# Optimization experiments

Hardware: AMD Instinct MI355X
Metric: run time of the kernel (lower is better)

The kernel has to match this reference:

```python
import jax, jax.numpy as jnp
import numpy as np

H = 2048

def setup_inputs() -> dict:
    key = jax.random.key(0)
    ks = jax.random.split(key, 7)
    s = 1.0 / np.sqrt(H)
    return {
        "input": jax.random.normal(ks[0], (2, 4096, H), dtype=jnp.float32),
        "Wq": jax.random.uniform(ks[1], (H, H), jnp.float32, -s, s),
        "bq": jax.random.uniform(ks[2], (H,), jnp.float32, -s, s),
        "Wk": jax.random.uniform(ks[3], (H, H), jnp.float32, -s, s),
        "bk": jax.random.uniform(ks[4], (H,), jnp.float32, -s, s),
        "Wv": jax.random.uniform(ks[5], (H, H), jnp.float32, -s, s),
        "bv": jax.random.uniform(ks[6], (H,), jnp.float32, -s, s),
    }

def reference(input, Wq, bq, Wk, bk, Wv, bv):
    # Linear projections: y = x @ W^T + b (torch nn.Linear convention)
    q = jnp.einsum('bsh,oh->bso', input, Wq) + bq
    k = jnp.einsum('bsh,oh->bso', input, Wk) + bk
    v = jnp.einsum('bsh,oh->bso', input, Wv) + bv
    # NOTE: original module has NO 1/sqrt(d) scaling and NO mask
    scores = jnp.einsum('bqh,bkh->bqk', q, k)          # [B,S,S]
    attn = jax.nn.softmax(scores, axis=-1)
    out = jnp.einsum('bqk,bkh->bqh', attn, v)           # [B,S,H]
    return out
```

## Files before the change

kernel.cpp:

```cpp
#include <hip/hip_runtime.h>
#include <hip/hip_bf16.h>
#include <cstdint>
#include <cstddef>


typedef _Float16 half8 __attribute__((ext_vector_type(8)));
typedef _Float16 half4 __attribute__((ext_vector_type(4)));
typedef float    f32x4 __attribute__((ext_vector_type(4)));

__device__ __forceinline__ void gld_lds16(const void* g, void* l) {
  __builtin_amdgcn_global_load_lds(
      (const __attribute__((address_space(1))) unsigned int*)g,
      (__attribute__((address_space(3))) unsigned int*)l, 16, 0, 0);
}

#define FENCE()  asm volatile("" ::: "memory")
#define LGKM(n)  asm volatile("s_waitcnt lgkmcnt(" #n ")" ::: "memory")
#define VMC(n)   asm volatile("s_waitcnt vmcnt(" #n ")" ::: "memory")
#define SBAR()   do { __builtin_amdgcn_s_barrier(); FENCE(); } while (0)
#define SCHED0() __builtin_amdgcn_sched_barrier(0)
#define PRIO1()  __builtin_amdgcn_s_setprio(1)
#define PRIO0()  __builtin_amdgcn_s_setprio(0)

#define LOAD_A(dst, RB, MH) do {                                            \
  const char* _p = ldsA + ((RB)*2 + wr) * 16384 + fr * 128;                 \
  _Pragma("unroll") for (int mi = 0; mi < 4; ++mi) {                        \
    dst[mi][0] = *(const half8*)(_p + ((MH)*4 + mi) * 2048 + cS0);          \
    dst[mi][1] = *(const half8*)(_p + ((MH)*4 + mi) * 2048 + cS1);          \
  }                                                                         \
} while (0)

#define LOAD_B(dst, RB, NH) do {                                            \
  const char* _p = ldsB + ((RB)*2 + (wc >> 1)) * 16384 +                    \
                   ((wc & 1) * 64 + fr) * 128;                              \
  _Pragma("unroll") for (int ni = 0; ni < 2; ++ni) {                        \
    dst[ni][0] = *(const half8*)(_p + ((NH)*2 + ni) * 2048 + cS0);          \
    dst[ni][1] = *(const half8*)(_p + ((NH)*2 + ni) * 2048 + cS1);          \
  }                                                                         \
} while (0)

#define MFMA_Q(AF, BF, MH, NH)                                              \
  _Pragma("unroll") for (int mi = 0; mi < 4; ++mi)                          \
  _Pragma("unroll") for (int ni = 0; ni < 2; ++ni) {                        \
    f32x4& _c = acc[(MH)*4 + mi][(NH)*2 + ni];                              \
    _c = __builtin_amdgcn_mfma_f32_16x16x32_f16(AF[mi][0], BF[ni][0], _c, 0, 0, 0); \
    _c = __builtin_amdgcn_mfma_f32_16x16x32_f16(AF[mi][1], BF[ni][1], _c, 0, 0, 0); \
  }

#define STAGE_A(bsel, h, kof)                                               \
  {                                                                         \
    const _Float16* _s = Abase + (size_t)((h) * 128) * lda + (kof);         \
    char* _d = ldsA + ((bsel)*2 + (h)) * 16384 + wvd;                       \
    gld_lds16(_s, _d);                                                      \
    gld_lds16(_s + lda8, _d + 1024);                                        \
  }
#define STAGE_B(bsel, h, kof)                                               \
  {                                                                         \
    const _Float16* _s = Bbase + (size_t)((h) * 128) * ldb + (kof);         \
    char* _d = ldsB + ((bsel)*2 + (h)) * 16384 + wvd;                       \
    gld_lds16(_s, _d);                                                      \
    gld_lds16(_s + ldb8, _d + 1024);                                        \
  }

template <int MODE>
__global__ __launch_bounds__(512) void gemm256(
    const _Float16* __restrict__ A, int lda,
    const _Float16* __restrict__ B, int ldb,
    const float* __restrict__ bias,
    void* __restrict__ out, int ldo, int K,
    size_t sA, size_t sB, size_t sO)
{
  __shared__ __attribute__((aligned(128))) char lds[131072];
  char* ldsA = (char*)lds;
  char* ldsB = (char*)lds + 65536;

  const int tid  = threadIdx.x;
  const int wv   = tid >> 6;
  const int lane = tid & 63;
  const int wr = wv >> 2;
  const int wc = wv & 3;
  const int bm = blockIdx.x * 256;
  const int bn = blockIdx.y * 256;
  A += (size_t)blockIdx.z * sA;
  B += (size_t)blockIdx.z * sB;

  const int fr = lane & 15;
  const int kq = lane >> 4;
  const int sx = (fr & 7) << 4;
  const int cS0 = (kq * 16) ^ sx;
  const int cS1 = (64 + kq * 16) ^ sx;
  const int lr  = lane >> 3;
  const int sc8 = ((lane & 7) ^ (lr & 7)) << 3;

  const _Float16* Abase = A + (size_t)(bm + wv * 16 + lr) * lda + sc8;
  const _Float16* Bbase = B + (size_t)(bn + wv * 16 + lr) * ldb + sc8;
  const size_t lda8 = (size_t)lda * 8, ldb8 = (size_t)ldb * 8;
  const int wvd = wv * 2048;

  f32x4 acc[8][4];
  const f32x4 zf = {0.f, 0.f, 0.f, 0.f};
#pragma unroll
  for (int mi = 0; mi < 8; ++mi)
#pragma unroll
    for (int ni = 0; ni < 4; ++ni) acc[mi][ni] = zf;

  half8 af[4][2], bf0[2][2], bf1[2][2];

  const int NT = K >> 6;
  const int NI = NT >> 1;

  STAGE_A(0, 0, 0); STAGE_A(0, 1, 0); STAGE_B(0, 0, 0); STAGE_B(0, 1, 0);
  STAGE_B(1, 0, 64); STAGE_B(1, 1, 64);
  VMC(4);
  SBAR();

  for (int it = 0; it < NI; ++it) {
    const bool more = (it < NI - 1);
    const size_t t1k = (size_t)(2 * it + 1) * 64;
    const size_t t2k = t1k + 64;
    const size_t t3k = t1k + 128;

    LOAD_A(af, 0, 0); LOAD_B(bf0, 0, 0);
    STAGE_A(1, 0, t1k);
    LGKM(8);
    SBAR(); LGKM(0); SCHED0();
    PRIO1(); MFMA_Q(af, bf0, 0, 0); PRIO0();
    SBAR();
    LOAD_B(bf1, 0, 1);
    STAGE_A(1, 1, t1k);
    SBAR(); LGKM(0); SCHED0();
    PRIO1(); MFMA_Q(af, bf1, 0, 1); PRIO0();
    SBAR();
    LOAD_A(af, 0, 1);
    if (more) STAGE_B(0, 0, t2k);
    SBAR(); LGKM(0); SCHED0();
    PRIO1(); MFMA_Q(af, bf1, 1, 1); PRIO0();
    SBAR();
    if (more) STAGE_B(0, 1, t2k);
    SBAR(); SCHED0();
    PRIO1(); MFMA_Q(af, bf0, 1, 0); PRIO0();
    if (more) { VMC(4); } else { VMC(0); }
    SBAR();

    LOAD_A(af, 1, 0); LOAD_B(bf0, 1, 0);
    if (more) STAGE_A(0, 0, t2k);
    LGKM(8);
    SBAR(); LGKM(0); SCHED0();
    PRIO1(); MFMA_Q(af, bf0, 0, 0); PRIO0();
    SBAR();
    LOAD_B(bf1, 1, 1);
    if (more) STAGE_A(0, 1, t2k);
    SBAR(); LGKM(0); SCHED0();
    PRIO1(); MFMA_Q(af, bf1, 0, 1); PRIO0();
    SBAR();
    LOAD_A(af, 1, 1);
    if (more) STAGE_B(1, 0, t3k);
    SBAR(); LGKM(0); SCHED0();
    PRIO1(); MFMA_Q(af, bf1, 1, 1); PRIO0();
    SBAR();
    if (more) STAGE_B(1, 1, t3k);
    SBAR(); SCHED0();
    PRIO1(); MFMA_Q(af, bf0, 1, 0); PRIO0();
    if (more) { VMC(4); } else { VMC(0); }
    SBAR();
  }

#pragma unroll
  for (int mi = 0; mi < 8; ++mi) {
#pragma unroll
    for (int ni = 0; ni < 4; ++ni) {
      const int col  = bn + wc * 64 + ni * 16 + fr;
      const int row0 = bm + wr * 128 + mi * 16 + kq * 4;
      const f32x4 a = acc[mi][ni];
      if constexpr (MODE == 0) {
        float* O = (float*)out + (size_t)blockIdx.z * sO;
#pragma unroll
        for (int j = 0; j < 4; ++j) O[(size_t)(row0 + j) * ldo + col] = a[j];
      } else if constexpr (MODE == 1) {
        _Float16* O = (_Float16*)out;
        const float bb = bias[col];
#pragma unroll
        for (int j = 0; j < 4; ++j)
          O[(size_t)(row0 + j) * ldo + col] = (_Float16)(a[j] + bb);
      } else if constexpr (MODE == 2) {
        _Float16* O = (_Float16*)out;
        const float bb = bias[col];
        half4 h;
#pragma unroll
        for (int j = 0; j < 4; ++j) h[j] = (_Float16)(a[j] + bb);
        *(half4*)(O + (size_t)col * ldo + row0) = h;
      } else {
        _Float16* O = (_Float16*)out + (size_t)blockIdx.z * sO;
#pragma unroll
        for (int j = 0; j < 4; ++j)
          O[(size_t)(row0 + j) * ldo + col] = (_Float16)a[j];
      }
    }
  }
}

__device__ __forceinline__ float wave_max_f(float v) {
#pragma unroll
  for (int o = 32; o; o >>= 1) v = fmaxf(v, __shfl_xor(v, o));
  return v;
}
__device__ __forceinline__ float wave_sum_f(float v) {
#pragma unroll
  for (int o = 32; o; o >>= 1) v += __shfl_xor(v, o);
  return v;
}

__global__ __launch_bounds__(256) void softmax_rows(
    const _Float16* __restrict__ S, _Float16* __restrict__ P)
{
  __shared__ float rmax[4], rsum[4];
  const int tid = threadIdx.x;
  const _Float16* s = S + (size_t)blockIdx.x * 4096;
  _Float16*       p = P + (size_t)blockIdx.x * 4096;

  const half8 v0 = ((const half8*)s)[tid];
  const half8 v1 = ((const half8*)s)[tid + 256];
  float f[16];
#pragma unroll
  for (int j = 0; j < 8; ++j) { f[j] = (float)v0[j]; f[8 + j] = (float)v1[j]; }

  float m = f[0];
#pragma unroll
  for (int j = 1; j < 16; ++j) m = fmaxf(m, f[j]);
  m = wave_max_f(m);
  if ((tid & 63) == 0) rmax[tid >> 6] = m;
  __syncthreads();
  m = fmaxf(fmaxf(rmax[0], rmax[1]), fmaxf(rmax[2], rmax[3]));

  float sum = 0.f;
#pragma unroll
  for (int j = 0; j < 16; ++j) { f[j] = __expf(f[j] - m); sum += f[j]; }
  sum = wave_sum_f(sum);
  if ((tid & 63) == 0) rsum[tid >> 6] = sum;
  __syncthreads();
  sum = rsum[0] + rsum[1] + rsum[2] + rsum[3];
  const float inv = 1.0f / sum;

  half8 o0, o1;
#pragma unroll
  for (int j = 0; j < 8; ++j) {
    o0[j] = (_Float16)(f[j] * inv);
    o1[j] = (_Float16)(f[8 + j] * inv);
  }
  ((half8*)p)[tid] = o0;
  ((half8*)p)[tid + 256] = o1;
}

__global__ __launch_bounds__(256) void cvt_f32_f16(
    const float* __restrict__ in, _Float16* __restrict__ out, int n4)
{
  const int stride = gridDim.x * 256;
  for (int idx = blockIdx.x * 256 + threadIdx.x; idx < n4; idx += stride) {
    const f32x4 x = ((const f32x4*)in)[idx];
    half4 h;
#pragma unroll
    for (int j = 0; j < 4; ++j) h[j] = (_Float16)x[j];
    ((half4*)out)[idx] = h;
  }
}

extern "C" void kernel_launch(void* const* d_in, const int* in_sizes, int n_in,
                              void* d_out, int out_size, void* d_ws, size_t ws_size,
                              hipStream_t stream)
{
  const float* X  = (const float*)d_in[0];
  const float* Wq = (const float*)d_in[1];
  const float* bq = (const float*)d_in[2];
  const float* Wk = (const float*)d_in[3];
  const float* bk = (const float*)d_in[4];
  const float* Wv = (const float*)d_in[5];
  const float* bv = (const float*)d_in[6];
  float* out = (float*)d_out;

  const size_t NX = (size_t)2 * 4096 * 2048;
  const size_t NW = (size_t)2048 * 2048;
  const size_t NS = (size_t)2 * 4096 * 4096;

  char* w = (char*)d_ws;
  _Float16* Ssc = (_Float16*)w;
  _Float16* Xh  = (_Float16*)w;
  _Float16* Wqh = (_Float16*)(w + NX * 2);
  _Float16* Wkh = (_Float16*)(w + NX * 2 + NW * 2);
  _Float16* Wvh = (_Float16*)(w + NX * 2 + 2 * NW * 2);
  _Float16* Q   = (_Float16*)(w + NS * 4);
  _Float16* Kp  = (_Float16*)(w + NS * 4 + NX * 2);
  _Float16* P   = (_Float16*)(w + NS * 4);
  _Float16* Vt  = (_Float16*)(w + NS * 4 + 2 * NX * 2);

  cvt_f32_f16<<<2048, 256, 0, stream>>>(X,  Xh,  (int)(NX / 4));
  cvt_f32_f16<<<512,  256, 0, stream>>>(Wq, Wqh, (int)(NW / 4));
  cvt_f32_f16<<<512,  256, 0, stream>>>(Wk, Wkh, (int)(NW / 4));
  cvt_f32_f16<<<512,  256, 0, stream>>>(Wv, Wvh, (int)(NW / 4));

  const dim3 blk(512);
  gemm256<1><<<dim3(32, 8, 1), blk, 0, stream>>>(Xh, 2048, Wqh, 2048, bq,
                                                 Q, 2048, 2048, 0, 0, 0);
  gemm256<1><<<dim3(32, 8, 1), blk, 0, stream>>>(Xh, 2048, Wkh, 2048, bk,
                                                 Kp, 2048, 2048, 0, 0, 0);
  gemm256<2><<<dim3(32, 8, 1), blk, 0, stream>>>(Xh, 2048, Wvh, 2048, bv,
                                                 Vt, 8192, 2048, 0, 0, 0);
  gemm256<3><<<dim3(16, 16, 2), blk, 0, stream>>>(
      Q, 2048, Kp, 2048, nullptr, Ssc, 4096, 2048,
      (size_t)4096 * 2048, (size_t)4096 * 2048, (size_t)4096 * 4096);
  softmax_rows<<<8192, 256, 0, stream>>>(Ssc, P);
  gemm256<0><<<dim3(16, 8, 2), blk, 0, stream>>>(
      P, 4096, Vt, 8192, nullptr, out, 2048, 4096,
      (size_t)4096 * 4096, (size_t)4096, (size_t)4096 * 2048);
}
```

Measured before the change: 489.8 us.

## Double-buffer register fragments to overlap LDS reads with MFMA in GEMM loop

Restructures the GEMM main loop so LDS fragment reads for the next quarter are issued before the current MFMA quarter, using extra A and B register fragment sets (afP/afQ, b0x/b0y). The explicit lgkmcnt waits are removed and the compiler is left to insert them, and the number of barriers per iteration is reduced. The next iteration's first fragments are prefetched before the loop ends. This aims to hide LDS latency behind matrix-core work and to cut synchronisation stalls. In exchange it uses more VGPRs and makes correctness depend on barrier placement relative to LDS buffer reuse.

```diff
diff --git a/kernel.cpp b/kernel.cpp
--- a/kernel.cpp
+++ b/kernel.cpp
@@ -15,7 +15,6 @@
 }
 
 #define FENCE()  asm volatile("" ::: "memory")
-#define LGKM(n)  asm volatile("s_waitcnt lgkmcnt(" #n ")" ::: "memory")
 #define VMC(n)   asm volatile("s_waitcnt vmcnt(" #n ")" ::: "memory")
 #define SBAR()   do { __builtin_amdgcn_s_barrier(); FENCE(); } while (0)
 #define SCHED0() __builtin_amdgcn_sched_barrier(0)
@@ -40,12 +39,14 @@
 } while (0)
 
 #define MFMA_Q(AF, BF, MH, NH)                                              \
+  PRIO1();                                                                  \
   _Pragma("unroll") for (int mi = 0; mi < 4; ++mi)                          \
   _Pragma("unroll") for (int ni = 0; ni < 2; ++ni) {                        \
     f32x4& _c = acc[(MH)*4 + mi][(NH)*2 + ni];                              \
     _c = __builtin_amdgcn_mfma_f32_16x16x32_f16(AF[mi][0], BF[ni][0], _c, 0, 0, 0); \
     _c = __builtin_amdgcn_mfma_f32_16x16x32_f16(AF[mi][1], BF[ni][1], _c, 0, 0, 0); \
-  }
+  }                                                                         \
+  PRIO0();
 
 #define STAGE_A(bsel, h, kof)                                               \
   {                                                                         \
@@ -104,7 +105,9 @@
 #pragma unroll
     for (int ni = 0; ni < 4; ++ni) acc[mi][ni] = zf;
 
-  half8 af[4][2], bf0[2][2], bf1[2][2];
+  half8 afP[4][2], afQ[4][2];
+  half8 b0x[2][2], b0y[2][2];
+  half8 b1[2][2];
 
   const int NT = K >> 6;
   const int NI = NT >> 1;
@@ -113,6 +116,9 @@
   STAGE_B(1, 0, 64); STAGE_B(1, 1, 64);
   VMC(4);
   SBAR();
+  LOAD_A(afP, 0, 0);
+  LOAD_B(b0x, 0, 0);
+  SCHED0();
 
   for (int it = 0; it < NI; ++it) {
     const bool more = (it < NI - 1);
@@ -120,49 +126,52 @@
     const size_t t2k = t1k + 64;
     const size_t t3k = t1k + 128;
 
-    LOAD_A(af, 0, 0); LOAD_B(bf0, 0, 0);
+    SBAR();
+    LOAD_B(b1, 0, 1);
     STAGE_A(1, 0, t1k);
-    LGKM(8);
-    SBAR(); LGKM(0); SCHED0();
-    PRIO1(); MFMA_Q(af, bf0, 0, 0); PRIO0();
-    SBAR();
-    LOAD_B(bf1, 0, 1);
+    SCHED0();
+    MFMA_Q(afP, b0x, 0, 0);
+    SBAR();
+    LOAD_A(afQ, 0, 1);
     STAGE_A(1, 1, t1k);
-    SBAR(); LGKM(0); SCHED0();
-    PRIO1(); MFMA_Q(af, bf1, 0, 1); PRIO0();
-    SBAR();
-    LOAD_A(af, 0, 1);
+    SCHED0();
+    MFMA_Q(afP, b1, 0, 1);
+    SBAR();
     if (more) STAGE_B(0, 0, t2k);
-    SBAR(); LGKM(0); SCHED0();
-    PRIO1(); MFMA_Q(af, bf1, 1, 1); PRIO0();
-    SBAR();
+    SCHED0();
+    MFMA_Q(afQ, b1, 1, 1);
+    if (more) { VMC(2); } else { VMC(0); }
+    SBAR();
+    LOAD_A(afP, 1, 0);
+    LOAD_B(b0y, 1, 0);
     if (more) STAGE_B(0, 1, t2k);
-    SBAR(); SCHED0();
-    PRIO1(); MFMA_Q(af, bf0, 1, 0); PRIO0();
-    if (more) { VMC(4); } else { VMC(0); }
-    SBAR();
-
-    LOAD_A(af, 1, 0); LOAD_B(bf0, 1, 0);
+    SCHED0();
+    MFMA_Q(afQ, b0x, 1, 0);
+    SBAR();
+    LOAD_B(b1, 1, 1);
     if (more) STAGE_A(0, 0, t2k);
-    LGKM(8);
-    SBAR(); LGKM(0); SCHED0();
-    PRIO1(); MFMA_Q(af, bf0, 0, 0); PRIO0();
-    SBAR();
-    LOAD_B(bf1, 1, 1);
+    SCHED0();
+    MFMA_Q(afP, b0y, 0, 0);
+    SBAR();
+    LOAD_A(afQ, 1, 1);
     if (more) STAGE_A(0, 1, t2k);
-    SBAR(); LGKM(0); SCHED0();
-    PRIO1(); MFMA_Q(af, bf1, 0, 1); PRIO0();
-    SBAR();
-    LOAD_A(af, 1, 1);
+    SCHED0();
+    MFMA_Q(afP, b1, 0, 1);
+    SBAR();
     if (more) STAGE_B(1, 0, t3k);
-    SBAR(); LGKM(0); SCHED0();
-    PRIO1(); MFMA_Q(af, bf1, 1, 1); PRIO0();
-    SBAR();
-    if (more) STAGE_B(1, 1, t3k);
-    SBAR(); SCHED0();
-    PRIO1(); MFMA_Q(af, bf0, 1, 0); PRIO0();
-    if (more) { VMC(4); } else { VMC(0); }
-    SBAR();
+    SCHED0();
+    MFMA_Q(afQ, b1, 1, 1);
+    if (more) {
+      VMC(2);
+      SBAR();
+      LOAD_A(afP, 0, 0);
+      LOAD_B(b0x, 0, 0);
+      STAGE_B(1, 1, t3k);
+      SCHED0();
+    } else {
+      SBAR();
+    }
+    MFMA_Q(afQ, b0y, 1, 0);
   }
 
 #pragma unroll
```

Result: slower. 826.9 us (+68.8%).

## Double-buffer A fragments and prefetch LDS reads ahead of MFMA phases

Applied to the files above, without the earlier changes.

Splits the A register fragments into two sets so the next A fragments are read from LDS while the current MFMA quarter runs, and loads both B fragment halves up front. The next iteration's first A fragment is prefetched at the end of the loop. The explicit lgkmcnt waits are dropped in favour of compiler-inserted ones, and the global-load wait moves to an earlier phase. The launch bound now requests 2 blocks per CU, which tightens the register budget and risks spilling given the large accumulator array.

```diff
diff --git a/kernel.cpp b/kernel.cpp
--- a/kernel.cpp
+++ b/kernel.cpp
@@ -15,7 +15,6 @@
 }
 
 #define FENCE()  asm volatile("" ::: "memory")
-#define LGKM(n)  asm volatile("s_waitcnt lgkmcnt(" #n ")" ::: "memory")
 #define VMC(n)   asm volatile("s_waitcnt vmcnt(" #n ")" ::: "memory")
 #define SBAR()   do { __builtin_amdgcn_s_barrier(); FENCE(); } while (0)
 #define SCHED0() __builtin_amdgcn_sched_barrier(0)
@@ -63,7 +62,7 @@
   }
 
 template <int MODE>
-__global__ __launch_bounds__(512) void gemm256(
+__global__ __launch_bounds__(512, 2) void gemm256(
     const _Float16* __restrict__ A, int lda,
     const _Float16* __restrict__ B, int ldb,
     const float* __restrict__ bias,
@@ -104,7 +103,7 @@
 #pragma unroll
     for (int ni = 0; ni < 4; ++ni) acc[mi][ni] = zf;
 
-  half8 af[4][2], bf0[2][2], bf1[2][2];
+  half8 afA[4][2], afB[4][2], b0[2][2], b1[2][2];
 
   const int NT = K >> 6;
   const int NI = NT >> 1;
@@ -113,6 +112,8 @@
   STAGE_B(1, 0, 64); STAGE_B(1, 1, 64);
   VMC(4);
   SBAR();
+  LOAD_A(afA, 0, 0);
+  SCHED0();
 
   for (int it = 0; it < NI; ++it) {
     const bool more = (it < NI - 1);
@@ -120,48 +121,45 @@
     const size_t t2k = t1k + 64;
     const size_t t3k = t1k + 128;
 
-    LOAD_A(af, 0, 0); LOAD_B(bf0, 0, 0);
+    LOAD_B(b0, 0, 0); LOAD_B(b1, 0, 1);
     STAGE_A(1, 0, t1k);
-    LGKM(8);
-    SBAR(); LGKM(0); SCHED0();
-    PRIO1(); MFMA_Q(af, bf0, 0, 0); PRIO0();
-    SBAR();
-    LOAD_B(bf1, 0, 1);
+    SBAR(); SCHED0();
+    PRIO1(); MFMA_Q(afA, b0, 0, 0); PRIO0();
+    SBAR();
+    LOAD_A(afB, 0, 1);
     STAGE_A(1, 1, t1k);
-    SBAR(); LGKM(0); SCHED0();
-    PRIO1(); MFMA_Q(af, bf1, 0, 1); PRIO0();
-    SBAR();
-    LOAD_A(af, 0, 1);
+    SBAR(); SCHED0();
+    PRIO1(); MFMA_Q(afA, b1, 0, 1); PRIO0();
+    SBAR();
     if (more) STAGE_B(0, 0, t2k);
-    SBAR(); LGKM(0); SCHED0();
-    PRIO1(); MFMA_Q(af, bf1, 1, 1); PRIO0();
-    SBAR();
+    SBAR(); SCHED0();
+    PRIO1(); MFMA_Q(afB, b1, 1, 1); PRIO0();
+    if (more) { VMC(2); } else { VMC(0); }
+    SBAR();
+    LOAD_A(afA, 1, 0);
     if (more) STAGE_B(0, 1, t2k);
     SBAR(); SCHED0();
-    PRIO1(); MFMA_Q(af, bf0, 1, 0); PRIO0();
-    if (more) { VMC(4); } else { VMC(0); }
-    SBAR();
-
-    LOAD_A(af, 1, 0); LOAD_B(bf0, 1, 0);
+    PRIO1(); MFMA_Q(afB, b0, 1, 0); PRIO0();
+    SBAR();
+
+    LOAD_B(b0, 1, 0); LOAD_B(b1, 1, 1);
     if (more) STAGE_A(0, 0, t2k);
-    LGKM(8);
-    SBAR(); LGKM(0); SCHED0();
-    PRIO1(); MFMA_Q(af, bf0, 0, 0); PRIO0();
-    SBAR();
-    LOAD_B(bf1, 1, 1);
+    SBAR(); SCHED0();
+    PRIO1(); MFMA_Q(afA, b0, 0, 0); PRIO0();
+    SBAR();
+    LOAD_A(afB, 1, 1);
     if (more) STAGE_A(0, 1, t2k);
-    SBAR(); LGKM(0); SCHED0();
-    PRIO1(); MFMA_Q(af, bf1, 0, 1); PRIO0();
-    SBAR();
-    LOAD_A(af, 1, 1);
+    SBAR(); SCHED0();
+    PRIO1(); MFMA_Q(afA, b1, 0, 1); PRIO0();
+    SBAR();
     if (more) STAGE_B(1, 0, t3k);
-    SBAR(); LGKM(0); SCHED0();
-    PRIO1(); MFMA_Q(af, bf1, 1, 1); PRIO0();
-    SBAR();
-    if (more) STAGE_B(1, 1, t3k);
-    SBAR(); SCHED0();
-    PRIO1(); MFMA_Q(af, bf0, 1, 0); PRIO0();
-    if (more) { VMC(4); } else { VMC(0); }
+    SBAR(); SCHED0();
+    PRIO1(); MFMA_Q(afB, b1, 1, 1); PRIO0();
+    if (more) { VMC(2); } else { VMC(0); }
+    SBAR();
+    if (more) { LOAD_A(afA, 0, 0); STAGE_B(1, 1, t3k); }
+    SBAR(); SCHED0();
+    PRIO1(); MFMA_Q(afB, b0, 1, 0); PRIO0();
     SBAR();
   }
 
```

Measured after the change: 517.2 us. +5.6%, slower.
